# Optimization experiments

Hardware: AMD Instinct MI355X
Metric: run time of the kernel (lower is better)

## Reference

```python
import jax, jax.numpy as jnp
import numpy as np

IN_CHANNELS = 128
N_NODES = 100000
N_EDGES = 625000


def setup_inputs() -> dict:
    key = jax.random.key(0)
    k1, k2, k3, k4, k5, k6 = jax.random.split(key, 6)
    d = IN_CHANNELS
    x = jax.random.normal(k1, (N_NODES, d), dtype=jnp.float32)
    edge_index = jax.random.randint(k2, (2, N_EDGES), 0, N_NODES, dtype=jnp.int64)
    # Linear params, torch default init: U(-1/sqrt(fan_in), 1/sqrt(fan_in))
    b1_bound = 1.0 / np.sqrt(2 * d)
    W1 = jax.random.uniform(k3, (d, 2 * d), minval=-b1_bound, maxval=b1_bound, dtype=jnp.float32)
    b1 = jax.random.uniform(k4, (d,), minval=-b1_bound, maxval=b1_bound, dtype=jnp.float32)
    b2_bound = 1.0 / np.sqrt(d)
    W2 = jax.random.uniform(k5, (1, d), minval=-b2_bound, maxval=b2_bound, dtype=jnp.float32)
    b2 = jax.random.uniform(k6, (1,), minval=-b2_bound, maxval=b2_bound, dtype=jnp.float32)
    return {"x": x, "edge_index": edge_index, "W1": W1, "b1": b1, "W2": W2, "b2": b2}


def reference(x, edge_index, W1, b1, W2, b2):
    # Gather endpoint features and concat along feature dim: [E, 2d]
    h = jnp.concatenate([x[edge_index[0]], x[edge_index[1]]], axis=1)
    h = jax.nn.relu(h @ W1.T + b1)          # [E, d]
    h = jax.nn.relu(h @ W2.T + b2)          # [E, 1]
    return jax.nn.sigmoid(h)
```

## Files before the change

### kernel.cpp

```cpp
#include <hip/hip_runtime.h>
#include <hip/hip_bf16.h>
#include <hip/hip_fp16.h>
#include <math.h>


typedef short    s16x4 __attribute__((ext_vector_type(4)));
typedef short    s16x8 __attribute__((ext_vector_type(8)));
typedef float    f32x2 __attribute__((ext_vector_type(2)));
typedef float    f32x4 __attribute__((ext_vector_type(4)));
typedef unsigned u32x4 __attribute__((ext_vector_type(4)));
typedef _Float16 h16x2 __attribute__((ext_vector_type(2)));

#define D 128

static __device__ inline short f2bf(float f) {
    unsigned u = __builtin_bit_cast(unsigned, f);
    unsigned r = (u + 0x7FFFu + ((u >> 16) & 1u)) >> 16;
    return (short)r;
}

static __device__ inline unsigned pkbf16(float a, float b) {
    unsigned r;
    asm("v_cvt_pk_bf16_f32 %0, %1, %2" : "=v"(r) : "v"(a), "v"(b));
    return r;
}

static __device__ inline unsigned enc2(float a, float b) {
#if __has_builtin(__builtin_amdgcn_cvt_pk_fp8_f32)
    return ((unsigned)__builtin_amdgcn_cvt_pk_fp8_f32(a, b, 0, false)) & 0xFFFFu;
#else
    unsigned r;
    asm("v_cvt_pk_fp8_f32 %0, %1, %2" : "=v"(r) : "v"(a), "v"(b));
    return r & 0xFFFFu;
#endif
}

#if __has_builtin(__builtin_amdgcn_cvt_pk_f16_fp8)
#define EDGE_PATH 0
#define YSC 1.0f
static __device__ inline h16x2 dec2lo(unsigned v) {
    return __builtin_amdgcn_cvt_pk_f16_fp8((short)v);
}
static __device__ inline h16x2 dec2hi(unsigned v) {
    return __builtin_amdgcn_cvt_pk_f16_fp8((short)(v >> 16));
}
static __device__ inline h16x2 reluh(h16x2 v) {
#if __has_builtin(__builtin_elementwise_max)
    h16x2 z = { (_Float16)0.0f, (_Float16)0.0f };
    return __builtin_elementwise_max(v, z);
#else
    unsigned u = __builtin_bit_cast(unsigned, v);
    unsigned m = ((u >> 15) & 0x00010001u) * 0xFFFFu;
    u &= ~m;
    return __builtin_bit_cast(h16x2, u);
#endif
}
static __device__ inline float dot2acc(h16x2 a, h16x2 b, float c) {
#if __has_builtin(__builtin_amdgcn_fdot2)
    return __builtin_amdgcn_fdot2(a, b, c, false);
#else
    return c + (float)a[0] * (float)b[0] + (float)a[1] * (float)b[1];
#endif
}
#else
#define EDGE_PATH 1
#if __has_builtin(__builtin_amdgcn_cvt_pk_f32_fp8)
static __device__ inline f32x2 d32lo(unsigned v) {
    return __builtin_amdgcn_cvt_pk_f32_fp8((int)v, false);
}
static __device__ inline f32x2 d32hi(unsigned v) {
    return __builtin_amdgcn_cvt_pk_f32_fp8((int)v, true);
}
#else
static __device__ inline f32x2 d32lo(unsigned v) {
    f32x2 r;
    asm("v_cvt_pk_f32_fp8 %0, %1" : "=v"(r) : "v"(v));
    return r;
}
static __device__ inline f32x2 d32hi(unsigned v) {
    f32x2 r;
    unsigned s = v >> 16;
    asm("v_cvt_pk_f32_fp8 %0, %1" : "=v"(r) : "v"(s));
    return r;
}
#endif
#endif

#define GRIDA 768

__global__ __launch_bounds__(256, 3) void precompute_kernel(
    const float* __restrict__ x,
    const float* __restrict__ W1,
    const float* __restrict__ b1,
    unsigned char* __restrict__ Y8,
    int N, int ntiles)
{
    const int tid  = threadIdx.x;
    const int wid  = tid >> 6;
    const int lane = tid & 63;
    const int quad = lane >> 4, l15 = lane & 15;
    const int cs   = wid;

    s16x8 bf[4][4];
    #pragma unroll
    for (int j = 0; j < 4; ++j) {
        #pragma unroll
        for (int c = 0; c < 4; ++c) {
            int o  = cs * 64 + j * 16 + l15;
            int kb = c * 32 + quad * 8;
            const float* wp = W1 + (size_t)(o & 127) * 256 + (o >> 7) * 128 + kb;
            f32x4 u0 = *(const f32x4*)wp;
            f32x4 u1 = *(const f32x4*)(wp + 4);
            u32x4 pk;
            pk[0] = pkbf16(u0[0], u0[1]);
            pk[1] = pkbf16(u0[2], u0[3]);
            pk[2] = pkbf16(u1[0], u1[1]);
            pk[3] = pkbf16(u1[2], u1[3]);
            bf[c][j] = __builtin_bit_cast(s16x8, pk);
        }
    }

    const bool qb0 = (quad & 1), qb1 = (quad & 2);

    for (int t = blockIdx.x; t < ntiles; t += GRIDA) {
        const int m0 = t * 32;

        f32x4 acc[2][4];
        #pragma unroll
        for (int j = 0; j < 4; ++j) {
            f32x4 bi = (cs < 2) ? *(const f32x4*)&b1[cs * 64 + j * 16 + quad * 4]
                                : (f32x4){0.f, 0.f, 0.f, 0.f};
            acc[0][j] = bi; acc[1][j] = bi;
        }

        #pragma unroll
        for (int i2 = 0; i2 < 2; ++i2) {
            int m = m0 + i2 * 16 + l15; if (m >= N) m = N - 1;
            const float* xr = x + (size_t)m * D + quad * 8;
            s16x8 af[4];
            #pragma unroll
            for (int c = 0; c < 4; ++c) {
                f32x4 lo = *(const f32x4*)(xr + c * 32);
                f32x4 hi = *(const f32x4*)(xr + c * 32 + 4);
                u32x4 pk;
                pk[0] = pkbf16(lo[0], lo[1]);
                pk[1] = pkbf16(lo[2], lo[3]);
                pk[2] = pkbf16(hi[0], hi[1]);
                pk[3] = pkbf16(hi[2], hi[3]);
                af[c] = __builtin_bit_cast(s16x8, pk);
            }
            #pragma unroll
            for (int c = 0; c < 4; ++c)
                #pragma unroll
                for (int j = 0; j < 4; ++j)
                    acc[i2][j] = __builtin_amdgcn_mfma_f32_16x16x32_bf16(
                        bf[c][j], af[c], acc[i2][j], 0, 0, 0);
        }

        #pragma unroll
        for (int i2 = 0; i2 < 2; ++i2) {
            unsigned dw[4];
            #pragma unroll
            for (int j = 0; j < 4; ++j) {
                f32x4 v = acc[i2][j];
                dw[j] = enc2(v[0], v[1]) | (enc2(v[2], v[3]) << 16);
            }
            unsigned s01 = qb0 ? dw[0] : dw[1];
            unsigned r01 = __shfl_xor(s01, 16);
            unsigned s23 = qb0 ? dw[2] : dw[3];
            unsigned r23 = __shfl_xor(s23, 16);
            unsigned a0 = qb0 ? r01 : dw[0];
            unsigned a1 = qb0 ? dw[1] : r01;
            unsigned a2 = qb0 ? r23 : dw[2];
            unsigned a3 = qb0 ? dw[3] : r23;
            unsigned s02 = qb1 ? a0 : a2;
            unsigned r02 = __shfl_xor(s02, 32);
            unsigned s13 = qb1 ? a1 : a3;
            unsigned r13 = __shfl_xor(s13, 32);
            uint4 ov;
            ov.x = qb1 ? r02 : a0;
            ov.y = qb1 ? r13 : a1;
            ov.z = qb1 ? a2 : r02;
            ov.w = qb1 ? a3 : r13;
            int m = m0 + i2 * 16 + l15;
            if (m < N)
                *(uint4*)(Y8 + (size_t)m * 256 + cs * 64 + quad * 16) = ov;
        }
    }
}

#define EPB 256

__global__ __launch_bounds__(256, 4) void edge_kernel(
    const unsigned char* __restrict__ Y8,
    const int*           __restrict__ ei,
    const float*         __restrict__ W2,
    const float*         __restrict__ b2,
    float*               __restrict__ out,
    int E)
{
    __shared__ int eis[2][EPB];

    const int tid = threadIdx.x;
    const int sub = tid & 7;
    const int grp = tid >> 3;
    const int e0b = blockIdx.x * EPB;

    {
        int e = e0b + tid;
        eis[0][tid] = (e < E) ? ei[e] : 0;
        eis[1][tid] = (e < E) ? ei[(size_t)E + e] : 0;
    }
    __syncthreads();

#if EDGE_PATH == 1
    f32x2 w2f[8];
    {
        const float* wp = &W2[sub * 16];
        #pragma unroll
        for (int q = 0; q < 8; ++q)
            w2f[q] = *(const f32x2*)(wp + q * 2);
    }
#else
    h16x2 w2h[8];
    {
        const float* wp = &W2[sub * 16];
        #pragma unroll
        for (int q = 0; q < 8; ++q) {
            float2 f = *(const float2*)(wp + q * 2);
            w2h[q] = (h16x2){ (_Float16)(f.x * YSC), (_Float16)(f.y * YSC) };
        }
    }
#endif

    uint4 L[8], R[8];
    #pragma unroll
    for (int k = 0; k < 8; ++k) {
        int ib  = grp + 32 * k;
        int src = eis[0][ib];
        int dst = eis[1][ib];
        L[k] = *(const uint4*)(Y8 + (size_t)src * 256 + sub * 16);
        R[k] = *(const uint4*)(Y8 + (size_t)dst * 256 + 128 + sub * 16);
    }

    float s[8] = { 0.f, 0.f, 0.f, 0.f, 0.f, 0.f, 0.f, 0.f };
    #pragma unroll
    for (int k = 0; k < 8; ++k) {
        const unsigned* a = (const unsigned*)&L[k];
        const unsigned* c = (const unsigned*)&R[k];
        #pragma unroll
        for (int d = 0; d < 4; ++d) {
#if EDGE_PATH == 1
            f32x2 zl = d32lo(a[d]) + d32lo(c[d]);
            f32x2 zh = d32hi(a[d]) + d32hi(c[d]);
            s[k] = fmaf(fmaxf(zl[0], 0.f), w2f[2*d][0], s[k]);
            s[k] = fmaf(fmaxf(zl[1], 0.f), w2f[2*d][1], s[k]);
            s[k] = fmaf(fmaxf(zh[0], 0.f), w2f[2*d + 1][0], s[k]);
            s[k] = fmaf(fmaxf(zh[1], 0.f), w2f[2*d + 1][1], s[k]);
#else
            h16x2 za = reluh(dec2lo(a[d]) + dec2lo(c[d]));
            s[k] = dot2acc(za, w2h[2*d],     s[k]);
            h16x2 zb = reluh(dec2hi(a[d]) + dec2hi(c[d]));
            s[k] = dot2acc(zb, w2h[2*d + 1], s[k]);
#endif
        }
    }

    #pragma unroll
    for (int k = 0; k < 8; ++k) {
        s[k] += __shfl_xor(s[k], 1);
        s[k] += __shfl_xor(s[k], 2);
        s[k] += __shfl_xor(s[k], 4);
    }

    if (sub == 0) {
        float bb = b2[0];
        #pragma unroll
        for (int k = 0; k < 8; ++k) {
            int e = e0b + grp + 32 * k;
            if (e < E) {
                float t = fmaxf(s[k] + bb, 0.f);
                out[e] = 1.0f / (1.0f + expf(-t));
            }
        }
    }
}

#define BM   128
#define BK   64
#define LDT  72

__global__ __launch_bounds__(256) void decoder_fallback_kernel(
    const float* __restrict__ x, const int* __restrict__ ei,
    const float* __restrict__ W1, const float* __restrict__ b1,
    const float* __restrict__ W2, const float* __restrict__ b2,
    float* __restrict__ out, int E)
{
    __shared__ int   nid[2][BM];
    __shared__ short At[BM * LDT];
    __shared__ short Bt[D * LDT];
    __shared__ float rowsum[BM][2];

    const int tid = threadIdx.x;
    const int e0  = blockIdx.x * BM;
    if (tid < BM) { int e = e0 + tid; nid[0][tid] = (e < E) ? ei[e] : 0; }
    else { int e = e0 + (tid - BM); nid[1][tid - BM] = (e < E) ? ei[E + e] : 0; }

    const int wid = tid >> 6, lane = tid & 63;
    const int wm = wid >> 1, wn = wid & 1;
    const int quad = lane >> 4, l15 = lane & 15;
    const int srow = tid >> 4, scol = (tid & 15) * 4;
    f32x4 acc[4][4] = {};
    __syncthreads();

    for (int t = 0; t < 4; ++t) {
        const int* ids = nid[t >> 1];
        const int kx = (t & 1) * BK, kw = t * BK;
        #pragma unroll
        for (int p = 0; p < 8; ++p) {
            int row = srow + p * 16;
            float4 v = *(const float4*)&x[(size_t)ids[row] * D + kx + scol];
            s16x4 bv = { f2bf(v.x), f2bf(v.y), f2bf(v.z), f2bf(v.w) };
            *(s16x4*)&At[row * LDT + scol] = bv;
        }
        #pragma unroll
        for (int p = 0; p < 8; ++p) {
            int n = srow + p * 16;
            float4 v = *(const float4*)&W1[n * 256 + kw + scol];
            s16x4 bv = { f2bf(v.x), f2bf(v.y), f2bf(v.z), f2bf(v.w) };
            *(s16x4*)&Bt[n * LDT + scol] = bv;
        }
        __syncthreads();
        #pragma unroll
        for (int c = 0; c < 2; ++c) {
            const int kc = c * 32;
            s16x8 af[4], bfr[4];
            #pragma unroll
            for (int i = 0; i < 4; ++i)
                af[i] = *(const s16x8*)&At[(wm*64 + i*16 + l15) * LDT + kc + quad*8];
            #pragma unroll
            for (int j = 0; j < 4; ++j)
                bfr[j] = *(const s16x8*)&Bt[(wn*64 + j*16 + l15) * LDT + kc + quad*8];
            #pragma unroll
            for (int i = 0; i < 4; ++i)
                #pragma unroll
                for (int j = 0; j < 4; ++j)
                    acc[i][j] = __builtin_amdgcn_mfma_f32_16x16x32_bf16(
                        af[i], bfr[j], acc[i][j], 0, 0, 0);
        }
        __syncthreads();
    }
    float b1v[4], w2v[4];
    #pragma unroll
    for (int j = 0; j < 4; ++j) {
        int col = wn*64 + j*16 + l15;
        b1v[j] = b1[col]; w2v[j] = W2[col];
    }
    float psum[16];
    #pragma unroll
    for (int t = 0; t < 16; ++t) psum[t] = 0.f;
    #pragma unroll
    for (int i = 0; i < 4; ++i)
        #pragma unroll
        for (int j = 0; j < 4; ++j)
            #pragma unroll
            for (int r = 0; r < 4; ++r) {
                float c = fmaxf(acc[i][j][r] + b1v[j], 0.f);
                psum[i*4 + r] += c * w2v[j];
            }
    #pragma unroll
    for (int off = 1; off < 16; off <<= 1)
        #pragma unroll
        for (int t = 0; t < 16; ++t)
            psum[t] += __shfl_xor(psum[t], off);
    if (l15 == 0) {
        #pragma unroll
        for (int i = 0; i < 4; ++i)
            #pragma unroll
            for (int r = 0; r < 4; ++r)
                rowsum[wm*64 + i*16 + quad*4 + r][wn] = psum[i*4 + r];
    }
    __syncthreads();
    if (tid < BM) {
        int e = e0 + tid;
        if (e < E) {
            float s = rowsum[tid][0] + rowsum[tid][1] + b2[0];
            s = fmaxf(s, 0.f);
            out[e] = 1.0f / (1.0f + expf(-s));
        }
    }
}

extern "C" void kernel_launch(void* const* d_in, const int* in_sizes, int n_in,
                              void* d_out, int out_size, void* d_ws, size_t ws_size,
                              hipStream_t stream) {
    const float* x  = (const float*)d_in[0];
    const int*   ei = (const int*)d_in[1];
    const float* W1 = (const float*)d_in[2];
    const float* b1 = (const float*)d_in[3];
    const float* W2 = (const float*)d_in[4];
    const float* b2 = (const float*)d_in[5];
    float* out = (float*)d_out;

    int E = in_sizes[1] / 2;
    int N = in_sizes[0] / D;

    size_t y_bytes = (size_t)N * 256;
    if (ws_size >= y_bytes) {
        unsigned char* Y8 = (unsigned char*)d_ws;
        int ntiles = (N + 31) / 32;
        int gridA  = (ntiles < GRIDA) ? ntiles : GRIDA;
        precompute_kernel<<<gridA, 256, 0, stream>>>(x, W1, b1, Y8, N, ntiles);
        int gridB = (E + EPB - 1) / EPB;
        edge_kernel<<<gridB, 256, 0, stream>>>(Y8, ei, W2, b2, out, E);
    } else {
        int nblocks = (E + BM - 1) / BM;
        decoder_fallback_kernel<<<nblocks, 256, 0, stream>>>(
            x, ei, W1, b1, W2, b2, out, E);
    }
}
```

Baseline: 152.2 us.

## Stage node-feature tiles into LDS with async triple-buffered prefetch

```diff
diff --git a/kernel.cpp b/kernel.cpp
--- a/kernel.cpp
+++ b/kernel.cpp
@@ -23,6 +23,12 @@
     unsigned r;
     asm("v_cvt_pk_bf16_f32 %0, %1, %2" : "=v"(r) : "v"(a), "v"(b));
     return r;
+}
+
+static __device__ inline void stage16(const void* g, void* l) {
+    __builtin_amdgcn_global_load_lds(
+        (const __attribute__((address_space(1))) void*)g,
+        (__attribute__((address_space(3))) void*)l, 16, 0, 0);
 }
 
 static __device__ inline unsigned enc2(float a, float b) {
@@ -95,6 +101,8 @@
     unsigned char* __restrict__ Y8,
     int N, int ntiles)
 {
+    __shared__ float Xt[3][32 * 128];
+
     const int tid  = threadIdx.x;
     const int wid  = tid >> 6;
     const int lane = tid & 63;
@@ -120,43 +128,83 @@
         }
     }
 
+    f32x4 b1v[4];
+    #pragma unroll
+    for (int j = 0; j < 4; ++j)
+        b1v[j] = (cs < 2) ? *(const f32x4*)&b1[cs * 64 + j * 16 + quad * 4]
+                          : (f32x4){0.f, 0.f, 0.f, 0.f};
+
+    const int rl   = wid * 2 + (lane >> 5);
+    const int colb = (lane & 31) * 16;
+    const char* xbytes = (const char*)x;
+
+    auto stage_tile = [&](int tt, int bb) {
+        char* lb = (char*)&Xt[bb][0] + wid * 1024;
+        #pragma unroll
+        for (int i = 0; i < 4; ++i) {
+            int row = i * 8 + rl;
+            int m = tt * 32 + row; if (m >= N) m = N - 1;
+            stage16(xbytes + (size_t)m * 512 + (colb ^ ((row & 7) << 4)),
+                    lb + i * 4096);
+        }
+    };
+
+    const int t0 = blockIdx.x;
+    if (t0 < ntiles)         stage_tile(t0, 0);
+    if (t0 + GRIDA < ntiles) stage_tile(t0 + GRIDA, 1);
+
+    const int swz = (l15 & 7) << 4;
     const bool qb0 = (quad & 1), qb1 = (quad & 2);
 
-    for (int t = blockIdx.x; t < ntiles; t += GRIDA) {
-        const int m0 = t * 32;
+    int it = 0;
+    for (int t = t0; t < ntiles; t += GRIDA, ++it) {
+        const bool hasnext = (t + GRIDA < ntiles);
+        if (it == 0) {
+            if (hasnext) asm volatile("s_waitcnt vmcnt(4)" ::: "memory");
+            else         asm volatile("s_waitcnt vmcnt(0)" ::: "memory");
+        } else {
+            if (hasnext) asm volatile("s_waitcnt vmcnt(6)" ::: "memory");
+            else         asm volatile("s_waitcnt vmcnt(2)" ::: "memory");
+        }
+        asm volatile("s_barrier" ::: "memory");
+
+        const int buf = it % 3;
 
         f32x4 acc[2][4];
         #pragma unroll
-        for (int j = 0; j < 4; ++j) {
-            f32x4 bi = (cs < 2) ? *(const f32x4*)&b1[cs * 64 + j * 16 + quad * 4]
-                                : (f32x4){0.f, 0.f, 0.f, 0.f};
-            acc[0][j] = bi; acc[1][j] = bi;
-        }
-
-        #pragma unroll
-        for (int i2 = 0; i2 < 2; ++i2) {
-            int m = m0 + i2 * 16 + l15; if (m >= N) m = N - 1;
-            const float* xr = x + (size_t)m * D + quad * 8;
-            s16x8 af[4];
-            #pragma unroll
-            for (int c = 0; c < 4; ++c) {
-                f32x4 lo = *(const f32x4*)(xr + c * 32);
-                f32x4 hi = *(const f32x4*)(xr + c * 32 + 4);
-                u32x4 pk;
-                pk[0] = pkbf16(lo[0], lo[1]);
-                pk[1] = pkbf16(lo[2], lo[3]);
-                pk[2] = pkbf16(hi[0], hi[1]);
-                pk[3] = pkbf16(hi[2], hi[3]);
-                af[c] = __builtin_bit_cast(s16x8, pk);
+        for (int j = 0; j < 4; ++j) { acc[0][j] = b1v[j]; acc[1][j] = b1v[j]; }
+
+        s16x8 af[2][4];
+        {
+            const char* xb8 = (const char*)&Xt[buf][0];
+            #pragma unroll
+            for (int i2 = 0; i2 < 2; ++i2) {
+                const char* rp = xb8 + (i2 * 16 + l15) * 512;
+                #pragma unroll
+                for (int c = 0; c < 4; ++c) {
+                    int kb = c * 128 + quad * 32;
+                    f32x4 lo = *(const f32x4*)(rp + ( kb       ^ swz));
+                    f32x4 hi = *(const f32x4*)(rp + ((kb + 16) ^ swz));
+                    u32x4 pk;
+                    pk[0] = pkbf16(lo[0], lo[1]);
+                    pk[1] = pkbf16(lo[2], lo[3]);
+                    pk[2] = pkbf16(hi[0], hi[1]);
+                    pk[3] = pkbf16(hi[2], hi[3]);
+                    af[i2][c] = __builtin_bit_cast(s16x8, pk);
+                }
             }
-            #pragma unroll
-            for (int c = 0; c < 4; ++c)
+        }
+
+        #pragma unroll
+        for (int c = 0; c < 4; ++c)
+            #pragma unroll
+            for (int i2 = 0; i2 < 2; ++i2)
                 #pragma unroll
                 for (int j = 0; j < 4; ++j)
                     acc[i2][j] = __builtin_amdgcn_mfma_f32_16x16x32_bf16(
-                        bf[c][j], af[c], acc[i2][j], 0, 0, 0);
-        }
-
+                        bf[c][j], af[i2][c], acc[i2][j], 0, 0, 0);
+
+        const int m0 = t * 32;
         #pragma unroll
         for (int i2 = 0; i2 < 2; ++i2) {
             unsigned dw[4];
@@ -186,6 +234,8 @@
             if (m < N)
                 *(uint4*)(Y8 + (size_t)m * 256 + cs * 64 + quad * 16) = ov;
         }
+
+        if (t + 2 * GRIDA < ntiles) stage_tile(t + 2 * GRIDA, (it + 2) % 3);
     }
 }
 
```

Measured after the change: 130.7 us. 1.16x faster.
